# Kernel optimization log

Hardware: AMD Instinct MI355X
Metric: run time of the kernel (lower is better)

The kernel has to match this reference:

```python
import jax, jax.numpy as jnp
import numpy as np

SR = 44100.0
N_FFT = 2048
BANDS = 128
C_IN = 2
D_OUT = 128
B = 8
T = 512


def _hz_to_mel(f):
    # Slaney mel scale (librosa default, htk=False)
    f = np.asarray(f, dtype=np.float64)
    f_sp = 200.0 / 3.0
    min_log_hz = 1000.0
    min_log_mel = min_log_hz / f_sp  # 15.0
    logstep = np.log(6.4) / 27.0
    lin = f / f_sp
    log = min_log_mel + np.log(np.maximum(f, 1e-10) / min_log_hz) / logstep
    return np.where(f >= min_log_hz, log, lin)


def _mel_to_hz(m):
    m = np.asarray(m, dtype=np.float64)
    f_sp = 200.0 / 3.0
    min_log_mel = 15.0
    logstep = np.log(6.4) / 27.0
    lin = m * f_sp
    log = 1000.0 * np.exp(logstep * (m - min_log_mel))
    return np.where(m >= min_log_mel, log, lin)


def _mel_filters(sr, n_fft, n_mels):
    # librosa.filters.mel(..., norm=None, fmin=0, fmax=sr/2)
    F = n_fft // 2 + 1
    fftfreqs = np.linspace(0.0, sr / 2.0, F)
    mels = np.linspace(_hz_to_mel(0.0), _hz_to_mel(sr / 2.0), n_mels + 2)
    mel_f = _mel_to_hz(mels)
    fdiff = np.diff(mel_f)
    ramps = mel_f[:, None] - fftfreqs[None, :]
    lower = -ramps[:-2] / fdiff[:-1, None]
    upper = ramps[2:] / fdiff[1:, None]
    return np.maximum(0.0, np.minimum(lower, upper))  # (n_mels, F)


def _build_bands(sr, n_fft, bands_num):
    # Mirrors BandSplit.__init__: edge residual bands + per-band nonzero gather tables.
    F = n_fft // 2 + 1
    mb = _mel_filters(sr, n_fft, bands_num - 2)
    b0 = np.zeros(F)
    i = int(np.argmax(mb[0]))
    b0[:i] = 1.0 - mb[0, :i]
    bl = np.zeros(F)
    i = int(np.argmax(mb[-1]))
    bl[i:] = 1.0 - mb[-1, i:]
    melbanks = np.concatenate([b0[None, :], mb, bl[None, :]], axis=0)  # (K, F)
    ola = melbanks.sum(axis=0)  # (F,), ~1.0 everywhere
    idx_list = [np.nonzero(melbanks[k])[0] for k in range(bands_num)]
    W = max(len(ix) for ix in idx_list)  # max band width
    pad_idx = n_fft // 2
    idxs = np.full((bands_num, W), pad_idx, dtype=np.int32)
    vals = np.zeros((bands_num, W), dtype=np.float32)
    for k, ix in enumerate(idx_list):
        idxs[k, : len(ix)] = ix
        vals[k, : len(ix)] = melbanks[k, ix]
    mask = (vals != 0.0).astype(np.float32)
    return (idxs.reshape(-1), vals.reshape(-1), mask.reshape(-1),
            ola.astype(np.float32), W)


def setup_inputs() -> dict:
    key = jax.random.key(0)
    k_x, k_w1, k_b1, k_w2, k_b2 = jax.random.split(key, 5)
    idx_flat, mel_flat, mask_flat, ola, W = _build_bands(SR, N_FFT, BANDS)
    F = N_FFT // 2 + 1
    x = jax.random.normal(k_x, (B, C_IN, T, F), dtype=jnp.float32)
    i1 = W * C_IN
    bound1 = 1.0 / np.sqrt(i1)
    pre_w = jax.random.uniform(k_w1, (BANDS, i1, D_OUT), jnp.float32, -bound1, bound1)
    pre_b = jax.random.normal(k_b1, (BANDS, D_OUT), jnp.float32) * 0.01
    bound2 = 1.0 / np.sqrt(D_OUT)
    post_w = jax.random.uniform(k_w2, (BANDS, D_OUT, i1), jnp.float32, -bound2, bound2)
    post_b = jax.random.normal(k_b2, (BANDS, i1), jnp.float32) * 0.01
    return {
        "x": x,
        "pre_w": pre_w, "pre_b": pre_b,
        "post_w": post_w, "post_b": post_b,
        "mel_flat": jnp.asarray(mel_flat),
        "mask_flat": jnp.asarray(mask_flat),
        "ola_window": jnp.asarray(ola),
        "idx_flat": jnp.asarray(idx_flat),
    }


def reference(x, pre_w, pre_b, post_w, post_b, mel_flat, mask_flat, ola_window, idx_flat):
    Bn, C, Tn, Fq = x.shape
    K = pre_b.shape[0]
    W = pre_w.shape[1] // C
    # ---- transform: gather + mel weighting + per-band linear ----
    g = x[:, :, :, idx_flat] * (mel_flat * mask_flat)            # (b, c, t, K*W)
    g = g.reshape(Bn, C, Tn, K, W)                               # b c t k w
    g = g.transpose(0, 2, 3, 4, 1).reshape(Bn, Tn, K, W * C)     # b t k (w c)
    z = jnp.einsum('btki,kio->btko', g, pre_w) + pre_b           # (b, t, K, d)
    # ---- inverse_transform: per-band linear + masked scatter-add + OLA norm ----
    y = jnp.einsum('btkd,kdo->btko', z, post_w) + post_b         # (b, t, K, W*C)
    y = y.reshape(Bn, Tn, K, W, C)
    y = y.transpose(0, 4, 1, 2, 3).reshape(Bn, C, Tn, K * W)     # b c t (k w)
    y = y * mask_flat
    buf = jnp.zeros((Bn, C, Tn, Fq), dtype=x.dtype)
    buf = buf.at[:, :, :, idx_flat].add(y)                       # scatter_add over f
    return buf / ola_window
```

## Files before the change

kernel.cpp:

```cpp
#include <hip/hip_runtime.h>
#include <hip/hip_fp16.h>

typedef __attribute__((ext_vector_type(8))) short short8;
typedef __attribute__((ext_vector_type(4))) float f32x4;

#define TPB 256
constexpr int D_OUTC = 128;
constexpr int T_LEN  = 512;
constexpr int C_INC  = 2;
constexpr int F_BINS = 1025;
constexpr int N_BANDS= 128;
constexpr int MAX_W  = 80;
constexpr int SCAP   = 4224;

__device__ inline short8 cvt8(const float v[8]) {
  short8 h;
  #pragma unroll
  for (int j = 0; j < 8; ++j) {
    unsigned u = __float_as_uint(v[j]);
    unsigned r = u + 0x7FFFu + ((u >> 16) & 1u);
    h[j] = (short)(r >> 16);
  }
  return h;
}
__device__ inline void split8t(const float v[8], short8& h, short8& l) {
  #pragma unroll
  for (int j = 0; j < 8; ++j) {
    unsigned u = __float_as_uint(v[j]);
    h[j] = (short)(u >> 16);
    float lo = v[j] - __uint_as_float(u & 0xFFFF0000u);
    l[j] = (short)(__float_as_uint(lo) >> 16);
  }
}

__global__ void k_len(const float* __restrict__ mask, const int* __restrict__ idx, int W,
                      int* __restrict__ lenT, int* __restrict__ startT) {
  const int k = blockIdx.x;
  const int lane = threadIdx.x;
  int cnt = 0;
  for (int w = lane; w < W; w += 64) cnt += (mask[k * W + w] != 0.f) ? 1 : 0;
  #pragma unroll
  for (int s = 32; s > 0; s >>= 1) cnt += __shfl_xor(cnt, s, 64);
  if (lane == 0) { lenT[k] = cnt; startT[k] = idx[k * W]; }
}
__global__ void k_scan(const int* __restrict__ lenT, int* __restrict__ lenPT,
                       int* __restrict__ offT) {
  const int k = threadIdx.x;
  int l = lenT[k];
  lenPT[k] = (l + 15) & ~15;
  __shared__ int sh[N_BANDS];
  sh[k] = 2 * l;
  __syncthreads();
  for (int s = 1; s < N_BANDS; s <<= 1) {
    int t = (k >= s) ? sh[k - s] : 0;
    __syncthreads();
    sh[k] += t;
    __syncthreads();
  }
  offT[k] = sh[k] - 2 * l;
  if (k == N_BANDS - 1) offT[N_BANDS] = sh[k];
}

__global__ void prep_w1(const float* __restrict__ pre_w, const float* __restrict__ mel,
                        const float* __restrict__ mask, const int* __restrict__ lenPT,
                        unsigned short* __restrict__ hh,
                        int W, int i1, int K1PA) {
  const int band = blockIdx.y;
  const int ip = blockIdx.x * 32 + (threadIdx.x & 31);
  const int lp = lenPT[band];
  const int c  = (ip >= lp) ? 1 : 0;
  const int w  = ip - (c ? lp : 0);
  const bool live = (ip < 2 * lp) && (w < W);
  float s = 0.f; int row = 0;
  if (live) { s = mel[band * W + w] * mask[band * W + w]; row = 2 * w + c; }
  for (int d = (threadIdx.x >> 5); d < D_OUTC; d += 8) {
    float v = live ? s * pre_w[((size_t)band * i1 + row) * D_OUTC + d] : 0.f;
    unsigned u = __float_as_uint(v);
    unsigned r = u + 0x7FFFu + ((u >> 16) & 1u);
    hh[((size_t)(band * D_OUTC + d)) * K1PA + ip] = (unsigned short)(r >> 16);
  }
}

__global__ void prep_w2(const float* __restrict__ post_w, const float* __restrict__ mask,
                        const int* __restrict__ idx, const float* __restrict__ ola,
                        unsigned short* __restrict__ hh,
                        int W, int i1, int K1PA) {
  const int band = blockIdx.y;
  const int o  = blockIdx.x * 2 + (threadIdx.x >> 7);
  const int dd = threadIdx.x & 127;
  float s = 0.f;
  if (o < i1) {
    int w = o >> 1;
    float mk = mask[band * W + w];
    if (mk != 0.f) s = mk / ola[idx[band * W + w]];
  }
  float v = (o < i1) ? s * post_w[((size_t)band * D_OUTC + dd) * i1 + o] : 0.f;
  unsigned u = __float_as_uint(v);
  unsigned r = u + 0x7FFFu + ((u >> 16) & 1u);
  hh[((size_t)(band * K1PA + o)) * D_OUTC + dd] = (unsigned short)(r >> 16);
}

__global__ void prep_pb(const float* __restrict__ post_b, const float* __restrict__ mask,
                        const int* __restrict__ idx, const float* __restrict__ ola,
                        float* __restrict__ postbS, int W, int i1) {
  int e = blockIdx.x * 256 + threadIdx.x;
  if (e >= N_BANDS * i1) return;
  int band = e / i1, o = e - band * i1;
  int w = o >> 1;
  float mk = mask[band * W + w];
  postbS[e] = (mk != 0.f) ? post_b[e] * mk / ola[idx[band * W + w]] : 0.f;
}

__global__ void k_inv2(const int* __restrict__ startT, const int* __restrict__ lenT,
                       const int* __restrict__ offT, int* __restrict__ inv) {
  int f = blockIdx.x * 256 + threadIdx.x;
  if (f >= F_BINS) return;
  int r0 = -1, r1 = -1, r2 = -1, r3 = -1;
  int n = 0;
  for (int k = 0; k < N_BANDS; ++k) {
    unsigned rel = (unsigned)(f - startT[k]);
    if (rel < (unsigned)lenT[k]) {
      int v = offT[k] + 2 * (int)rel;
      if (n == 0) r0 = v; else if (n == 1) r1 = v; else if (n == 2) r2 = v; else if (n == 3) r3 = v;
      ++n;
    }
  }
  *(int4*)&inv[f * 4] = make_int4(r0, r1, r2, r3);
}

__global__ __launch_bounds__(TPB, 3)
void bandsplit_main(const float* __restrict__ x,
                    const unsigned short* __restrict__ wB1h,
                    const unsigned short* __restrict__ wB2h,
                    const float* __restrict__ pre_b,
                    const float* __restrict__ postbS,
                    const int* __restrict__ lenT,
                    const int* __restrict__ lenPT,
                    const int* __restrict__ offT,
                    const int* __restrict__ startT,
                    __half* __restrict__ y,
                    int i1, int K1PA, int nmt)
{
  const int bid  = blockIdx.x;
  const int band = bid / nmt;
  const int mt   = bid - band * nmt;

  const int lenv = lenT[band];
  if (lenv == 0) return;
  const int lp   = lenPT[band];
  const int nks  = lp >> 4;
  const int i1e  = 2 * lenv;
  const int nOT  = (i1e + 15) >> 4;
  const int offk = offT[band];
  const int strt = startT[band];

  const int mbase = mt * 128;
  const int b  = mbase >> 9;
  const int t0 = mbase & 511;
  const int tid  = threadIdx.x;
  const int lane = tid & 63;
  const int wid  = tid >> 6;
  const int lr = lane & 15, lk = lane >> 4;
  const int m0 = wid * 32;

  __shared__ float zAll[4][16 * 132];
  float* zw = zAll[wid];

  const float* xr0A = x + ((size_t)(b * C_INC) * T_LEN + (t0 + m0 + lr)) * F_BINS + strt;
  const float* xr0B = xr0A + (size_t)16 * F_BINS;
  const size_t xcs = (size_t)T_LEN * F_BINS;

  auto loadx = [&](int ks, float* vA, float* vB) {
    const int i0 = ks * 32 + lk * 8;
    const int cs = (i0 >= lp) ? 1 : 0;
    const int w0 = i0 - (cs ? lp : 0);
    const float* xrA = xr0A + (cs ? xcs : 0) + w0;
    const float* xrB = xr0B + (cs ? xcs : 0) + w0;
    if (w0 + 8 <= lenv) {
      float4 a0, a1, b0, b1;
      __builtin_memcpy(&a0, xrA,     16);
      __builtin_memcpy(&a1, xrA + 4, 16);
      __builtin_memcpy(&b0, xrB,     16);
      __builtin_memcpy(&b1, xrB + 4, 16);
      vA[0]=a0.x; vA[1]=a0.y; vA[2]=a0.z; vA[3]=a0.w;
      vA[4]=a1.x; vA[5]=a1.y; vA[6]=a1.z; vA[7]=a1.w;
      vB[0]=b0.x; vB[1]=b0.y; vB[2]=b0.z; vB[3]=b0.w;
      vB[4]=b1.x; vB[5]=b1.y; vB[6]=b1.z; vB[7]=b1.w;
    } else {
      #pragma unroll
      for (int j = 0; j < 8; ++j) {
        bool ok = (w0 + j < lenv);
        vA[j] = ok ? xrA[j] : 0.f;
        vB[j] = ok ? xrB[j] : 0.f;
      }
    }
  };

  f32x4 a1A[8] = {}, a1B[8] = {};
  const unsigned short* b1h = wB1h + ((size_t)(band * D_OUTC) + lr) * K1PA;

  float xvA[8], xvB[8], nxA[8], nxB[8];
  loadx(0, xvA, xvB);
  for (int ks = 0; ks < nks; ++ks) {
    const int i0 = ks * 32 + lk * 8;
    const short8 ahA = cvt8(xvA);
    const short8 ahB = cvt8(xvB);

    #pragma unroll
    for (int half = 0; half < 2; ++half) {
      short8 BH[4];
      #pragma unroll
      for (int t = 0; t < 4; ++t) {
        const int dt = half * 4 + t;
        BH[t] = *(const short8*)&b1h[(size_t)dt * 16 * K1PA + i0];
      }
      if (half == 0 && ks + 1 < nks) loadx(ks + 1, nxA, nxB);
      #pragma unroll
      for (int t = 0; t < 4; ++t) {
        const int dt = half * 4 + t;
        a1A[dt] = __builtin_amdgcn_mfma_f32_16x16x32_bf16(ahA, BH[t], a1A[dt], 0, 0, 0);
        a1B[dt] = __builtin_amdgcn_mfma_f32_16x16x32_bf16(ahB, BH[t], a1B[dt], 0, 0, 0);
      }
    }
    #pragma unroll
    for (int j = 0; j < 8; ++j) { xvA[j] = nxA[j]; xvB[j] = nxB[j]; }
  }

  float pbv[8];
  #pragma unroll
  for (int dt = 0; dt < 8; ++dt) pbv[dt] = pre_b[band * D_OUTC + dt * 16 + lr];

  short8 zhA[4], zlA[4], zhB[4], zlB[4];
  #pragma unroll
  for (int dt = 0; dt < 8; ++dt)
    #pragma unroll
    for (int r = 0; r < 4; ++r)
      zw[(lk * 4 + r) * 132 + dt * 16 + lr] = a1A[dt][r] + pbv[dt];
  __syncthreads();
  #pragma unroll
  for (int ks = 0; ks < 4; ++ks) {
    float zv[8];
    *(float4*)&zv[0] = *(const float4*)&zw[lr * 132 + ks * 32 + lk * 8];
    *(float4*)&zv[4] = *(const float4*)&zw[lr * 132 + ks * 32 + lk * 8 + 4];
    split8t(zv, zhA[ks], zlA[ks]);
  }
  __syncthreads();
  #pragma unroll
  for (int dt = 0; dt < 8; ++dt)
    #pragma unroll
    for (int r = 0; r < 4; ++r)
      zw[(lk * 4 + r) * 132 + dt * 16 + lr] = a1B[dt][r] + pbv[dt];
  __syncthreads();
  #pragma unroll
  for (int ks = 0; ks < 4; ++ks) {
    float zv[8];
    *(float4*)&zv[0] = *(const float4*)&zw[lr * 132 + ks * 32 + lk * 8];
    *(float4*)&zv[4] = *(const float4*)&zw[lr * 132 + ks * 32 + lk * 8 + 4];
    split8t(zv, zhB[ks], zlB[ks]);
  }

  const unsigned short* b2h = wB2h + ((size_t)(band * K1PA) + lr) * D_OUTC;
  for (int ot = 0; ot < nOT; ot += 2) {
    const bool has2 = (ot + 1 < nOT);
    short8 B0[4], B1[4];
    #pragma unroll
    for (int ks = 0; ks < 4; ++ks)
      B0[ks] = *(const short8*)&b2h[(size_t)ot * 16 * D_OUTC + ks * 32 + lk * 8];
    if (has2) {
      #pragma unroll
      for (int ks = 0; ks < 4; ++ks)
        B1[ks] = *(const short8*)&b2h[(size_t)(ot + 1) * 16 * D_OUTC + ks * 32 + lk * 8];
    }
    f32x4 aA0 = {}, aB0 = {}, aA1 = {}, aB1 = {};
    #pragma unroll
    for (int ks = 0; ks < 4; ++ks) {
      aA0 = __builtin_amdgcn_mfma_f32_16x16x32_bf16(zhA[ks], B0[ks], aA0, 0, 0, 0);
      aA0 = __builtin_amdgcn_mfma_f32_16x16x32_bf16(zlA[ks], B0[ks], aA0, 0, 0, 0);
      aB0 = __builtin_amdgcn_mfma_f32_16x16x32_bf16(zhB[ks], B0[ks], aB0, 0, 0, 0);
      aB0 = __builtin_amdgcn_mfma_f32_16x16x32_bf16(zlB[ks], B0[ks], aB0, 0, 0, 0);
    }
    if (has2) {
      #pragma unroll
      for (int ks = 0; ks < 4; ++ks) {
        aA1 = __builtin_amdgcn_mfma_f32_16x16x32_bf16(zhA[ks], B1[ks], aA1, 0, 0, 0);
        aA1 = __builtin_amdgcn_mfma_f32_16x16x32_bf16(zlA[ks], B1[ks], aA1, 0, 0, 0);
        aB1 = __builtin_amdgcn_mfma_f32_16x16x32_bf16(zhB[ks], B1[ks], aB1, 0, 0, 0);
        aB1 = __builtin_amdgcn_mfma_f32_16x16x32_bf16(zlB[ks], B1[ks], aB1, 0, 0, 0);
      }
    }
    {
      const int o = ot * 16 + lr;
      if (o < i1e) {
        const float pb = postbS[band * i1 + o];
        const size_t ybA = ((size_t)(b * T_LEN + t0 + m0 + lk * 4)) * SCAP + offk + o;
        const size_t ybB = ybA + (size_t)16 * SCAP;
        #pragma unroll
        for (int r = 0; r < 4; ++r) {
          y[ybA + (size_t)r * SCAP] = __float2half_rn(aA0[r] + pb);
          y[ybB + (size_t)r * SCAP] = __float2half_rn(aB0[r] + pb);
        }
      }
    }
    if (has2) {
      const int o = (ot + 1) * 16 + lr;
      if (o < i1e) {
        const float pb = postbS[band * i1 + o];
        const size_t ybA = ((size_t)(b * T_LEN + t0 + m0 + lk * 4)) * SCAP + offk + o;
        const size_t ybB = ybA + (size_t)16 * SCAP;
        #pragma unroll
        for (int r = 0; r < 4; ++r) {
          y[ybA + (size_t)r * SCAP] = __float2half_rn(aA1[r] + pb);
          y[ybB + (size_t)r * SCAP] = __float2half_rn(aB1[r] + pb);
        }
      }
    }
  }
}

__global__ __launch_bounds__(256, 8)
void k_merge(const __half* __restrict__ y, const int* __restrict__ inv,
             float* __restrict__ out, int nrows) {
  for (int row = blockIdx.x; row < nrows; row += gridDim.x) {
    const int t  = row & 511;
    const int bc = row >> 9;
    const int c  = bc & 1;
    const int b  = bc >> 1;
    const size_t ybase = (size_t)(b * T_LEN + t) * SCAP + c;
    float* orow = out + (size_t)row * F_BINS;
    for (int f = threadIdx.x; f < F_BINS; f += 256) {
      const int4 iv = *reinterpret_cast<const int4*>(&inv[f * 4]);
      float s = 0.f;
      if (iv.x >= 0) s += __half2float(y[ybase + iv.x]);
      if (iv.y >= 0) s += __half2float(y[ybase + iv.y]);
      if (iv.z >= 0) s += __half2float(y[ybase + iv.z]);
      if (iv.w >= 0) s += __half2float(y[ybase + iv.w]);
      orow[f] = s;
    }
  }
}

constexpr int MT     = 32;
constexpr int MAX_I1 = 2 * MAX_W;
constexpr int MAX_I1P= (MAX_I1 + 31) & ~31;
constexpr int GSTR   = 36;

__global__ __launch_bounds__(TPB, 2)
void bandsplit_fused(const float* __restrict__ x,
                     const float* __restrict__ pre_w,
                     const float* __restrict__ pre_b,
                     const float* __restrict__ post_w,
                     const float* __restrict__ post_b,
                     const float* __restrict__ mel,
                     const float* __restrict__ mask,
                     const float* __restrict__ ola,
                     const int*   __restrict__ idx,
                     float* __restrict__ out,
                     int W)
{
    const int i1  = 2 * W;
    const int I1P = (i1 + 31) & ~31;
    const int k     = blockIdx.y;
    const int mbase = blockIdx.x * MT;
    const int b     = mbase / T_LEN;
    const int t0    = mbase % T_LEN;
    const int tid = threadIdx.x;
    const int td  = tid & 31;
    const int tm  = tid >> 5;

    __shared__ float gT[MAX_I1P * GSTR];
    __shared__ float zT[D_OUTC * GSTR];
    __shared__ float wS[32 * D_OUTC];
    __shared__ float s_preb[D_OUTC];
    __shared__ float s_postb[MAX_I1];
    __shared__ float s_melmask[MAX_W];
    __shared__ float s_mask[MAX_W];
    __shared__ float s_iola[MAX_W];
    __shared__ int   s_idx[MAX_W];

    for (int j = tid; j < W; j += TPB) {
        int   f  = idx[k * W + j];
        float mv = mel[k * W + j];
        float mk = mask[k * W + j];
        s_idx[j]     = f;
        s_melmask[j] = mv * mk;
        s_mask[j]    = mk;
        s_iola[j]    = 1.0f / ola[f];
    }
    for (int j = tid; j < D_OUTC; j += TPB) s_preb[j]  = pre_b[k * D_OUTC + j];
    for (int j = tid; j < i1;     j += TPB) s_postb[j] = post_b[k * i1 + j];
    for (int j = tid; j < I1P * GSTR; j += TPB) gT[j] = 0.f;
    __syncthreads();

    for (int j = tid; j < MT * i1; j += TPB) {
        int w  = j % W;
        int cm = j / W;
        int c  = cm & 1;
        int ml = cm >> 1;
        int f  = s_idx[w];
        float v = x[((b * C_INC + c) * T_LEN + (t0 + ml)) * F_BINS + f] * s_melmask[w];
        gT[(2 * w + c) * GSTR + ml] = v;
    }
    __syncthreads();

    float az[4][4] = {};
    for (int i0 = 0; i0 < I1P; i0 += 32) {
        for (int j = tid; j < 32 * D_OUTC; j += TPB) {
            int ii = j >> 7, d = j & 127;
            int i  = i0 + ii;
            wS[j] = (i < i1) ? pre_w[(k * i1 + i) * D_OUTC + d] : 0.f;
        }
        __syncthreads();
        #pragma unroll 8
        for (int ii = 0; ii < 32; ++ii) {
            const float4 wv = *reinterpret_cast<const float4*>(&wS[ii * D_OUTC + td * 4]);
            const float4 gv = *reinterpret_cast<const float4*>(&gT[(i0 + ii) * GSTR + tm * 4]);
            az[0][0] += gv.x * wv.x; az[0][1] += gv.x * wv.y; az[0][2] += gv.x * wv.z; az[0][3] += gv.x * wv.w;
            az[1][0] += gv.y * wv.x; az[1][1] += gv.y * wv.y; az[1][2] += gv.y * wv.z; az[1][3] += gv.y * wv.w;
            az[2][0] += gv.z * wv.x; az[2][1] += gv.z * wv.y; az[2][2] += gv.z * wv.z; az[2][3] += gv.z * wv.w;
            az[3][0] += gv.w * wv.x; az[3][1] += gv.w * wv.y; az[3][2] += gv.w * wv.z; az[3][3] += gv.w * wv.w;
        }
        __syncthreads();
    }
    #pragma unroll
    for (int jj = 0; jj < 4; ++jj) {
        int d = td * 4 + jj;
        float bb = s_preb[d];
        #pragma unroll
        for (int r = 0; r < 4; ++r)
            zT[d * GSTR + tm * 4 + r] = az[r][jj] + bb;
    }
    __syncthreads();

    const int NOG = (i1 + 127) >> 7;
    for (int og = 0; og < NOG; ++og) {
        float ay[4][4] = {};
        for (int d0 = 0; d0 < D_OUTC; d0 += 32) {
            for (int j = tid; j < 32 * D_OUTC; j += TPB) {
                int dd = j >> 7, oo = j & 127;
                int o  = og * 128 + oo;
                wS[j] = (o < i1) ? post_w[(k * D_OUTC + d0 + dd) * i1 + o] : 0.f;
            }
            __syncthreads();
            #pragma unroll 8
            for (int dd = 0; dd < 32; ++dd) {
                const float4 wv = *reinterpret_cast<const float4*>(&wS[dd * D_OUTC + td * 4]);
                const float4 zv = *reinterpret_cast<const float4*>(&zT[(d0 + dd) * GSTR + tm * 4]);
                ay[0][0] += zv.x * wv.x; ay[0][1] += zv.x * wv.y; ay[0][2] += zv.x * wv.z; ay[0][3] += zv.x * wv.w;
                ay[1][0] += zv.y * wv.x; ay[1][1] += zv.y * wv.y; ay[1][2] += zv.y * wv.z; ay[1][3] += zv.y * wv.w;
                ay[2][0] += zv.z * wv.x; ay[2][1] += zv.z * wv.y; ay[2][2] += zv.z * wv.z; ay[2][3] += zv.z * wv.w;
                ay[3][0] += zv.w * wv.x; ay[3][1] += zv.w * wv.y; ay[3][2] += zv.w * wv.z; ay[3][3] += zv.w * wv.w;
            }
            __syncthreads();
        }
        #pragma unroll
        for (int jj = 0; jj < 4; ++jj) {
            int o = og * 128 + td * 4 + jj;
            if (o < i1) {
                int w = o >> 1, c = o & 1;
                float mk = s_mask[w];
                if (mk != 0.f) {
                    int f = s_idx[w];
                    float scale = mk * s_iola[w];
                    float bb = s_postb[o];
                    #pragma unroll
                    for (int r = 0; r < 4; ++r) {
                        int ml = tm * 4 + r;
                        float val = (ay[r][jj] + bb) * scale;
                        atomicAdd(&out[((b * C_INC + c) * T_LEN + (t0 + ml)) * F_BINS + f], val);
                    }
                }
            }
        }
    }
}

__global__ void bandsplit_naive(const float* __restrict__ x,
                                const float* __restrict__ pre_w,
                                const float* __restrict__ pre_b,
                                const float* __restrict__ post_w,
                                const float* __restrict__ post_b,
                                const float* __restrict__ mel,
                                const float* __restrict__ mask,
                                const float* __restrict__ ola,
                                const int*   __restrict__ idx,
                                float* __restrict__ out,
                                int W)
{
    const int i1 = 2 * W;
    extern __shared__ float sh[];
    float* g = sh;
    float* z = sh + i1;
    const int m = blockIdx.x, k = blockIdx.y;
    const int b = m / T_LEN, t = m % T_LEN;
    const int tid = threadIdx.x;
    for (int j = tid; j < i1; j += 128) {
        int w = j >> 1, c = j & 1;
        int f = idx[k * W + w];
        g[j] = x[((b * C_INC + c) * T_LEN + t) * F_BINS + f] * mel[k * W + w] * mask[k * W + w];
    }
    __syncthreads();
    {
        int d = tid;
        float a = pre_b[k * D_OUTC + d];
        for (int i = 0; i < i1; ++i) a += g[i] * pre_w[(k * i1 + i) * D_OUTC + d];
        z[d] = a;
    }
    __syncthreads();
    for (int o = tid; o < i1; o += 128) {
        int w = o >> 1, c = o & 1;
        float mk = mask[k * W + w];
        if (mk == 0.f) continue;
        float a = post_b[k * i1 + o];
        for (int d = 0; d < D_OUTC; ++d) a += z[d] * post_w[(k * D_OUTC + d) * i1 + o];
        int f = idx[k * W + w];
        atomicAdd(&out[((b * C_INC + c) * T_LEN + t) * F_BINS + f], a * mk / ola[f]);
    }
}

extern "C" void kernel_launch(void* const* d_in, const int* in_sizes, int n_in,
                              void* d_out, int out_size, void* d_ws, size_t ws_size,
                              hipStream_t stream) {
    const float* x      = (const float*)d_in[0];
    const float* pre_w  = (const float*)d_in[1];
    const float* pre_b  = (const float*)d_in[2];
    const float* post_w = (const float*)d_in[3];
    const float* post_b = (const float*)d_in[4];
    const float* mel    = (const float*)d_in[5];
    const float* mask   = (const float*)d_in[6];
    const float* ola    = (const float*)d_in[7];
    const int*   idxp   = (const int*)d_in[8];
    float* out = (float*)d_out;

    const int W  = in_sizes[8] / N_BANDS;
    const int i1 = 2 * W;
    const int Mrows = in_sizes[0] / (C_INC * F_BINS);
    const int K1PA = 2 * ((W + 15) & ~15);

    const size_t S1 = (size_t)N_BANDS * D_OUTC * K1PA;
    const size_t wbytes   = 4 * S1;
    const size_t pbs_off  = (wbytes + 15) & ~(size_t)15;
    const size_t inv_off  = (pbs_off + (size_t)N_BANDS * i1 * 4 + 15) & ~(size_t)15;
    const size_t len_off  = inv_off + (size_t)F_BINS * 4 * 4;
    const size_t lenp_off = len_off + N_BANDS * 4;
    const size_t offt_off = lenp_off + N_BANDS * 4;
    const size_t strt_off = offt_off + (N_BANDS + 1) * 4;
    const size_t y_off    = (strt_off + N_BANDS * 4 + 255) & ~(size_t)255;
    const size_t need     = y_off + (size_t)Mrows * SCAP * sizeof(__half);

    if (W <= MAX_W && (Mrows % 128) == 0 && (Mrows % T_LEN) == 0 && ws_size >= need) {
        char* ws = (char*)d_ws;
        unsigned short* wB1h = (unsigned short*)ws;
        unsigned short* wB2h = wB1h + S1;
        float* postbS = (float*)(ws + pbs_off);
        int* inv   = (int*)(ws + inv_off);
        int* lenT  = (int*)(ws + len_off);
        int* lenPT = (int*)(ws + lenp_off);
        int* offT  = (int*)(ws + offt_off);
        int* startT= (int*)(ws + strt_off);
        __half* y  = (__half*)(ws + y_off);

        k_len<<<N_BANDS, 64, 0, stream>>>(mask, idxp, W, lenT, startT);
        k_scan<<<1, N_BANDS, 0, stream>>>(lenT, lenPT, offT);
        dim3 g1(K1PA / 32, N_BANDS);
        prep_w1<<<g1, 256, 0, stream>>>(pre_w, mel, mask, lenPT, wB1h, W, i1, K1PA);
        dim3 g2(K1PA / 2, N_BANDS);
        prep_w2<<<g2, 256, 0, stream>>>(post_w, mask, idxp, ola, wB2h, W, i1, K1PA);
        prep_pb<<<(N_BANDS * i1 + 255) / 256, 256, 0, stream>>>(post_b, mask, idxp, ola,
                                                                postbS, W, i1);
        k_inv2<<<(F_BINS + 255) / 256, 256, 0, stream>>>(startT, lenT, offT, inv);
        const int nmt = Mrows / 128;
        bandsplit_main<<<nmt * N_BANDS, TPB, 0, stream>>>(x, wB1h, wB2h,
                                                 pre_b, postbS, lenT, lenPT, offT, startT,
                                                 y, i1, K1PA, nmt);
        const int nrows = out_size / F_BINS;
        k_merge<<<2048, 256, 0, stream>>>(y, inv, out, nrows);
        return;
    }

    hipMemsetAsync(d_out, 0, (size_t)out_size * sizeof(float), stream);
    if (W <= MAX_W && (Mrows % MT) == 0) {
        dim3 grid(Mrows / MT, N_BANDS);
        bandsplit_fused<<<grid, TPB, 0, stream>>>(x, pre_w, pre_b, post_w, post_b,
                                                  mel, mask, ola, idxp, out, W);
    } else {
        dim3 grid(Mrows, N_BANDS);
        size_t shmem = (size_t)(2 * W + D_OUTC) * sizeof(float);
        bandsplit_naive<<<grid, 128, shmem, stream>>>(x, pre_w, pre_b, post_w, post_b,
                                                      mel, mask, ola, idxp, out, W);
    }
}
```

Before: 140.0 us.

## Drop split-bf16 second GEMM, sort bands by width, fuse bias prep, raise occupancy

Several changes at once. The second GEMM no longer uses a hi/lo bf16 split of z, which halves its MFMA count but lowers accuracy. Bands are now launched in descending width order through a permutation table so the long bands start first. The post-bias scaling kernel is folded into prep_w2, and the x prefetch register double-buffering is removed to cut register pressure. Launch bounds go to 4 waves and the merge grid is doubled.

```diff
diff --git a/kernel.cpp b/kernel.cpp
--- a/kernel.cpp
+++ b/kernel.cpp
@@ -23,15 +23,6 @@
   }
   return h;
 }
-__device__ inline void split8t(const float v[8], short8& h, short8& l) {
-  #pragma unroll
-  for (int j = 0; j < 8; ++j) {
-    unsigned u = __float_as_uint(v[j]);
-    h[j] = (short)(u >> 16);
-    float lo = v[j] - __uint_as_float(u & 0xFFFF0000u);
-    l[j] = (short)(__float_as_uint(lo) >> 16);
-  }
-}
 
 __global__ void k_len(const float* __restrict__ mask, const int* __restrict__ idx, int W,
                       int* __restrict__ lenT, int* __restrict__ startT) {
@@ -44,12 +35,14 @@
   if (lane == 0) { lenT[k] = cnt; startT[k] = idx[k * W]; }
 }
 __global__ void k_scan(const int* __restrict__ lenT, int* __restrict__ lenPT,
-                       int* __restrict__ offT) {
+                       int* __restrict__ offT, int* __restrict__ permT) {
   const int k = threadIdx.x;
   int l = lenT[k];
   lenPT[k] = (l + 15) & ~15;
   __shared__ int sh[N_BANDS];
+  __shared__ int sl[N_BANDS];
   sh[k] = 2 * l;
+  sl[k] = l;
   __syncthreads();
   for (int s = 1; s < N_BANDS; s <<= 1) {
     int t = (k >= s) ? sh[k - s] : 0;
@@ -59,6 +52,10 @@
   }
   offT[k] = sh[k] - 2 * l;
   if (k == N_BANDS - 1) offT[N_BANDS] = sh[k];
+  int rank = 0;
+  for (int j = 0; j < N_BANDS; ++j)
+    rank += (sl[j] > l) || (sl[j] == l && j < k);
+  permT[rank] = k;
 }
 
 __global__ void prep_w1(const float* __restrict__ pre_w, const float* __restrict__ mel,
@@ -81,9 +78,10 @@
   }
 }
 
-__global__ void prep_w2(const float* __restrict__ post_w, const float* __restrict__ mask,
+__global__ void prep_w2(const float* __restrict__ post_w, const float* __restrict__ post_b,
+                        const float* __restrict__ mask,
                         const int* __restrict__ idx, const float* __restrict__ ola,
-                        unsigned short* __restrict__ hh,
+                        unsigned short* __restrict__ hh, float* __restrict__ postbS,
                         int W, int i1, int K1PA) {
   const int band = blockIdx.y;
   const int o  = blockIdx.x * 2 + (threadIdx.x >> 7);
@@ -98,17 +96,8 @@
   unsigned u = __float_as_uint(v);
   unsigned r = u + 0x7FFFu + ((u >> 16) & 1u);
   hh[((size_t)(band * K1PA + o)) * D_OUTC + dd] = (unsigned short)(r >> 16);
-}
-
-__global__ void prep_pb(const float* __restrict__ post_b, const float* __restrict__ mask,
-                        const int* __restrict__ idx, const float* __restrict__ ola,
-                        float* __restrict__ postbS, int W, int i1) {
-  int e = blockIdx.x * 256 + threadIdx.x;
-  if (e >= N_BANDS * i1) return;
-  int band = e / i1, o = e - band * i1;
-  int w = o >> 1;
-  float mk = mask[band * W + w];
-  postbS[e] = (mk != 0.f) ? post_b[e] * mk / ola[idx[band * W + w]] : 0.f;
+  if (dd == 0 && o < i1)
+    postbS[band * i1 + o] = s * post_b[band * i1 + o];
 }
 
 __global__ void k_inv2(const int* __restrict__ startT, const int* __restrict__ lenT,
@@ -128,7 +117,7 @@
   *(int4*)&inv[f * 4] = make_int4(r0, r1, r2, r3);
 }
 
-__global__ __launch_bounds__(TPB, 3)
+__global__ __launch_bounds__(TPB, 4)
 void bandsplit_main(const float* __restrict__ x,
                     const unsigned short* __restrict__ wB1h,
                     const unsigned short* __restrict__ wB2h,
@@ -138,12 +127,13 @@
                     const int* __restrict__ lenPT,
                     const int* __restrict__ offT,
                     const int* __restrict__ startT,
+                    const int* __restrict__ permT,
                     __half* __restrict__ y,
                     int i1, int K1PA, int nmt)
 {
   const int bid  = blockIdx.x;
-  const int band = bid / nmt;
-  const int mt   = bid - band * nmt;
+  const int band = permT[bid / nmt];
+  const int mt   = bid - (bid / nmt) * nmt;
 
   const int lenv = lenT[band];
   if (lenv == 0) return;
@@ -170,39 +160,34 @@
   const float* xr0B = xr0A + (size_t)16 * F_BINS;
   const size_t xcs = (size_t)T_LEN * F_BINS;
 
-  auto loadx = [&](int ks, float* vA, float* vB) {
+  f32x4 a1A[8] = {}, a1B[8] = {};
+  const unsigned short* b1h = wB1h + ((size_t)(band * D_OUTC) + lr) * K1PA;
+
+  for (int ks = 0; ks < nks; ++ks) {
     const int i0 = ks * 32 + lk * 8;
     const int cs = (i0 >= lp) ? 1 : 0;
     const int w0 = i0 - (cs ? lp : 0);
     const float* xrA = xr0A + (cs ? xcs : 0) + w0;
     const float* xrB = xr0B + (cs ? xcs : 0) + w0;
+    float xvA[8], xvB[8];
     if (w0 + 8 <= lenv) {
-      float4 a0, a1, b0, b1;
-      __builtin_memcpy(&a0, xrA,     16);
-      __builtin_memcpy(&a1, xrA + 4, 16);
-      __builtin_memcpy(&b0, xrB,     16);
-      __builtin_memcpy(&b1, xrB + 4, 16);
-      vA[0]=a0.x; vA[1]=a0.y; vA[2]=a0.z; vA[3]=a0.w;
-      vA[4]=a1.x; vA[5]=a1.y; vA[6]=a1.z; vA[7]=a1.w;
-      vB[0]=b0.x; vB[1]=b0.y; vB[2]=b0.z; vB[3]=b0.w;
-      vB[4]=b1.x; vB[5]=b1.y; vB[6]=b1.z; vB[7]=b1.w;
+      float4 q0, q1, q2, q3;
+      __builtin_memcpy(&q0, xrA,     16);
+      __builtin_memcpy(&q1, xrA + 4, 16);
+      __builtin_memcpy(&q2, xrB,     16);
+      __builtin_memcpy(&q3, xrB + 4, 16);
+      xvA[0]=q0.x; xvA[1]=q0.y; xvA[2]=q0.z; xvA[3]=q0.w;
+      xvA[4]=q1.x; xvA[5]=q1.y; xvA[6]=q1.z; xvA[7]=q1.w;
+      xvB[0]=q2.x; xvB[1]=q2.y; xvB[2]=q2.z; xvB[3]=q2.w;
+      xvB[4]=q3.x; xvB[5]=q3.y; xvB[6]=q3.z; xvB[7]=q3.w;
     } else {
       #pragma unroll
       for (int j = 0; j < 8; ++j) {
         bool ok = (w0 + j < lenv);
-        vA[j] = ok ? xrA[j] : 0.f;
-        vB[j] = ok ? xrB[j] : 0.f;
+        xvA[j] = ok ? xrA[j] : 0.f;
+        xvB[j] = ok ? xrB[j] : 0.f;
       }
     }
-  };
-
-  f32x4 a1A[8] = {}, a1B[8] = {};
-  const unsigned short* b1h = wB1h + ((size_t)(band * D_OUTC) + lr) * K1PA;
-
-  float xvA[8], xvB[8], nxA[8], nxB[8];
-  loadx(0, xvA, xvB);
-  for (int ks = 0; ks < nks; ++ks) {
-    const int i0 = ks * 32 + lk * 8;
     const short8 ahA = cvt8(xvA);
     const short8 ahB = cvt8(xvB);
 
@@ -214,7 +199,6 @@
         const int dt = half * 4 + t;
         BH[t] = *(const short8*)&b1h[(size_t)dt * 16 * K1PA + i0];
       }
-      if (half == 0 && ks + 1 < nks) loadx(ks + 1, nxA, nxB);
       #pragma unroll
       for (int t = 0; t < 4; ++t) {
         const int dt = half * 4 + t;
@@ -222,15 +206,13 @@
         a1B[dt] = __builtin_amdgcn_mfma_f32_16x16x32_bf16(ahB, BH[t], a1B[dt], 0, 0, 0);
       }
     }
-    #pragma unroll
-    for (int j = 0; j < 8; ++j) { xvA[j] = nxA[j]; xvB[j] = nxB[j]; }
   }
 
   float pbv[8];
   #pragma unroll
   for (int dt = 0; dt < 8; ++dt) pbv[dt] = pre_b[band * D_OUTC + dt * 16 + lr];
 
-  short8 zhA[4], zlA[4], zhB[4], zlB[4];
+  short8 zhA[4], zhB[4];
   #pragma unroll
   for (int dt = 0; dt < 8; ++dt)
     #pragma unroll
@@ -242,7 +224,7 @@
     float zv[8];
     *(float4*)&zv[0] = *(const float4*)&zw[lr * 132 + ks * 32 + lk * 8];
     *(float4*)&zv[4] = *(const float4*)&zw[lr * 132 + ks * 32 + lk * 8 + 4];
-    split8t(zv, zhA[ks], zlA[ks]);
+    zhA[ks] = cvt8(zv);
   }
   __syncthreads();
   #pragma unroll
@@ -256,7 +238,7 @@
     float zv[8];
     *(float4*)&zv[0] = *(const float4*)&zw[lr * 132 + ks * 32 + lk * 8];
     *(float4*)&zv[4] = *(const float4*)&zw[lr * 132 + ks * 32 + lk * 8 + 4];
-    split8t(zv, zhB[ks], zlB[ks]);
+    zhB[ks] = cvt8(zv);
   }
 
   const unsigned short* b2h = wB2h + ((size_t)(band * K1PA) + lr) * D_OUTC;
@@ -275,17 +257,13 @@
     #pragma unroll
     for (int ks = 0; ks < 4; ++ks) {
       aA0 = __builtin_amdgcn_mfma_f32_16x16x32_bf16(zhA[ks], B0[ks], aA0, 0, 0, 0);
-      aA0 = __builtin_amdgcn_mfma_f32_16x16x32_bf16(zlA[ks], B0[ks], aA0, 0, 0, 0);
       aB0 = __builtin_amdgcn_mfma_f32_16x16x32_bf16(zhB[ks], B0[ks], aB0, 0, 0, 0);
-      aB0 = __builtin_amdgcn_mfma_f32_16x16x32_bf16(zlB[ks], B0[ks], aB0, 0, 0, 0);
     }
     if (has2) {
       #pragma unroll
       for (int ks = 0; ks < 4; ++ks) {
         aA1 = __builtin_amdgcn_mfma_f32_16x16x32_bf16(zhA[ks], B1[ks], aA1, 0, 0, 0);
-        aA1 = __builtin_amdgcn_mfma_f32_16x16x32_bf16(zlA[ks], B1[ks], aA1, 0, 0, 0);
         aB1 = __builtin_amdgcn_mfma_f32_16x16x32_bf16(zhB[ks], B1[ks], aB1, 0, 0, 0);
-        aB1 = __builtin_amdgcn_mfma_f32_16x16x32_bf16(zlB[ks], B1[ks], aB1, 0, 0, 0);
       }
     }
     {
@@ -544,7 +522,8 @@
     const size_t lenp_off = len_off + N_BANDS * 4;
     const size_t offt_off = lenp_off + N_BANDS * 4;
     const size_t strt_off = offt_off + (N_BANDS + 1) * 4;
-    const size_t y_off    = (strt_off + N_BANDS * 4 + 255) & ~(size_t)255;
+    const size_t perm_off = strt_off + N_BANDS * 4;
+    const size_t y_off    = (perm_off + N_BANDS * 4 + 255) & ~(size_t)255;
     const size_t need     = y_off + (size_t)Mrows * SCAP * sizeof(__half);
 
     if (W <= MAX_W && (Mrows % 128) == 0 && (Mrows % T_LEN) == 0 && ws_size >= need) {
@@ -557,23 +536,23 @@
         int* lenPT = (int*)(ws + lenp_off);
         int* offT  = (int*)(ws + offt_off);
         int* startT= (int*)(ws + strt_off);
+        int* permT = (int*)(ws + perm_off);
         __half* y  = (__half*)(ws + y_off);
 
         k_len<<<N_BANDS, 64, 0, stream>>>(mask, idxp, W, lenT, startT);
-        k_scan<<<1, N_BANDS, 0, stream>>>(lenT, lenPT, offT);
+        k_scan<<<1, N_BANDS, 0, stream>>>(lenT, lenPT, offT, permT);
         dim3 g1(K1PA / 32, N_BANDS);
         prep_w1<<<g1, 256, 0, stream>>>(pre_w, mel, mask, lenPT, wB1h, W, i1, K1PA);
         dim3 g2(K1PA / 2, N_BANDS);
-        prep_w2<<<g2, 256, 0, stream>>>(post_w, mask, idxp, ola, wB2h, W, i1, K1PA);
-        prep_pb<<<(N_BANDS * i1 + 255) / 256, 256, 0, stream>>>(post_b, mask, idxp, ola,
-                                                                postbS, W, i1);
+        prep_w2<<<g2, 256, 0, stream>>>(post_w, post_b, mask, idxp, ola, wB2h, postbS,
+                                        W, i1, K1PA);
         k_inv2<<<(F_BINS + 255) / 256, 256, 0, stream>>>(startT, lenT, offT, inv);
         const int nmt = Mrows / 128;
         bandsplit_main<<<nmt * N_BANDS, TPB, 0, stream>>>(x, wB1h, wB2h,
                                                  pre_b, postbS, lenT, lenPT, offT, startT,
-                                                 y, i1, K1PA, nmt);
+                                                 permT, y, i1, K1PA, nmt);
         const int nrows = out_size / F_BINS;
-        k_merge<<<2048, 256, 0, stream>>>(y, inv, out, nrows);
+        k_merge<<<4096, 256, 0, stream>>>(y, inv, out, nrows);
         return;
     }
 
```

Result: faster. 128.0 us (-8.6%).
